# Kernel tuning notes

Hardware: AMD Instinct MI355X
Metric: run time of the kernel (lower is better)

The kernel has to match this reference:

```python
import jax, jax.numpy as jnp
import numpy as np

IOU_THRES = 0.45
NEG_POS_RATIO = 3
BBOX_XFORM_CLIP = float(np.log(1000.0 / 16.0))  # torchvision BoxCoder clamp


def _make_boxes(key, shape, img=512.0):
    # valid xyxy boxes inside a 512x512 image
    k1, k2 = jax.random.split(key)
    cxy = jax.random.uniform(k1, shape + (2,), minval=32.0, maxval=img - 32.0)
    wh = jax.random.uniform(k2, shape + (2,), minval=8.0, maxval=128.0)
    return jnp.concatenate([cxy - 0.5 * wh, cxy + 0.5 * wh], axis=-1)


def setup_inputs() -> dict:
    key = jax.random.key(0)
    B, A, G, C = 32, 32768, 64, 91
    ks = jax.random.split(key, 5)
    return {
        "cls_logits": jax.random.normal(ks[0], (B, A, C), dtype=jnp.float32),
        "bbox_regression": 0.1 * jax.random.normal(ks[1], (B, A, 4), dtype=jnp.float32),
        "anchors": _make_boxes(ks[2], (B, A)),
        "gt_boxes": _make_boxes(ks[3], (B, G)),
        "gt_labels": jax.random.randint(ks[4], (B, G), 0, C - 1),  # fg classes; C-1 is background
    }


def _pairwise_iou(boxes, anchors):
    # boxes [B,G,4] xyxy, anchors [B,A,4] xyxy -> [B,G,A]
    b = boxes[:, :, None, :]
    a = anchors[:, None, :, :]
    tl = jnp.maximum(b[..., :2], a[..., :2])
    br = jnp.minimum(b[..., 2:], a[..., 2:])
    wh = jnp.clip(br - tl, 0.0)
    inter = wh[..., 0] * wh[..., 1]
    area_b = (b[..., 2] - b[..., 0]) * (b[..., 3] - b[..., 1])
    area_a = (a[..., 2] - a[..., 0]) * (a[..., 3] - a[..., 1])
    return inter / (area_b + area_a - inter + 1e-16)


def _match(ious):
    # SSDMatcher: per-anchor best gt, threshold, then force best anchor per gt.
    # ious [G,A] -> matches [A] in {-1, 0..G-1}
    G = ious.shape[0]
    vals = ious.max(axis=0)
    m = jnp.argmax(ious, axis=0)
    m = jnp.where(vals < IOU_THRES, -1, m)
    best_anchor_per_gt = jnp.argmax(ious, axis=1)  # [G]
    return m.at[best_anchor_per_gt].set(jnp.arange(G))


def _decode(reg, anchors):
    # torchvision BoxCoder.decode_single, weights (1,1,1,1), xyxy anchors
    w = anchors[..., 2] - anchors[..., 0]
    h = anchors[..., 3] - anchors[..., 1]
    cx = anchors[..., 0] + 0.5 * w
    cy = anchors[..., 1] + 0.5 * h
    dx, dy, dw, dh = reg[..., 0], reg[..., 1], reg[..., 2], reg[..., 3]
    dw = jnp.minimum(dw, BBOX_XFORM_CLIP)
    dh = jnp.minimum(dh, BBOX_XFORM_CLIP)
    pcx = dx * w + cx
    pcy = dy * h + cy
    pw = jnp.exp(dw) * w
    ph = jnp.exp(dh) * h
    return jnp.stack([pcx - 0.5 * pw, pcy - 0.5 * ph, pcx + 0.5 * pw, pcy + 0.5 * ph], axis=-1)


def _giou_loss(pred, gt):
    # GIoU loss on xyxy boxes; elementwise over leading dims
    tl = jnp.maximum(pred[..., :2], gt[..., :2])
    br = jnp.minimum(pred[..., 2:], gt[..., 2:])
    wh = jnp.clip(br - tl, 0.0)
    inter = wh[..., 0] * wh[..., 1]
    ap = (pred[..., 2] - pred[..., 0]) * (pred[..., 3] - pred[..., 1])
    ag = (gt[..., 2] - gt[..., 0]) * (gt[..., 3] - gt[..., 1])
    union = ap + ag - inter + 1e-16
    iou = inter / union
    ctl = jnp.minimum(pred[..., :2], gt[..., :2])
    cbr = jnp.maximum(pred[..., 2:], gt[..., 2:])
    cwh = cbr - ctl
    ac = cwh[..., 0] * cwh[..., 1]
    giou = iou - (ac - union) / jnp.clip(ac, 1e-16)
    return 1.0 - jnp.clip(giou, -1.0, 1.0)


def reference(cls_logits, bbox_regression, anchors, gt_boxes, gt_labels):
    B, A, C = cls_logits.shape
    # --- matching ---
    ious = _pairwise_iou(gt_boxes, anchors)        # [B,G,A]
    matched = jax.vmap(_match)(ious)               # [B,A]
    fg = matched >= 0                              # [B,A]
    idx = jnp.clip(matched, 0)
    num_fg = fg.sum()
    # --- bbox loss (sum over foreground only, via masking) ---
    matched_gt = jnp.take_along_axis(gt_boxes, idx[..., None], axis=1)  # [B,A,4]
    pred = _decode(bbox_regression, anchors)                            # [B,A,4]
    bbox_loss_sum = jnp.sum(_giou_loss(pred, matched_gt) * fg)
    # --- classification targets + CE ---
    matched_lbl = jnp.take_along_axis(gt_labels, idx, axis=1)           # [B,A]
    cls_targets = jnp.where(fg, matched_lbl, C - 1)
    logp = jax.nn.log_softmax(cls_logits, axis=-1)
    cls_loss = -jnp.take_along_axis(logp, cls_targets[..., None], axis=-1)[..., 0]  # [B,A]
    neg_loss = jnp.where(fg, -jnp.inf, cls_loss)
    order = jnp.argsort(-neg_loss, axis=1)         # descending
    rank = jnp.argsort(order, axis=1)
    num_neg = NEG_POS_RATIO * fg.sum(axis=1, keepdims=True)
    bg = rank < num_neg
    # --- normalize ---
    N = jnp.maximum(1, num_fg).astype(cls_loss.dtype)
    bbox_loss = 2.0 * bbox_loss_sum / N
    cls_total = (jnp.sum(cls_loss * fg) + jnp.sum(cls_loss * bg)) / N
    return jnp.stack([bbox_loss, cls_total])  # [bbox_loss, cls_loss]
```

## Files before the change

### kernel.cpp

```cpp
#include <hip/hip_runtime.h>
#include <hip/hip_bf16.h>

#define B 32
#define A 32768
#define G 64
#define C 91
#define NBINS 2048

typedef unsigned long long ull;

static constexpr size_t offMatched = 0;
static constexpr size_t offBits    = (size_t)B * A * 4;
static constexpr size_t offNumFg   = (size_t)2 * B * A * 4;
static constexpr size_t offAcc     = offNumFg + B * 4;
static constexpr size_t offTick    = offAcc + 3 * 8;
static constexpr size_t offGt      = offTick + 8;
static constexpr int    ZERO_N     = (int)((offGt - offNumFg) / 4);

__global__ void init_kernel(int* zero_base, ull* gtpack) {
  int i = blockIdx.x * 256 + threadIdx.x;
  if (i < ZERO_N) zero_base[i] = 0;
  if (i < B * G) gtpack[i] = 0xFFFFFFFFull;
}

__global__ __launch_bounds__(256) void match_kernel(
    const float4* __restrict__ anchors, const float4* __restrict__ gt_boxes,
    int* __restrict__ matched, ull* __restrict__ gtpack) {
#pragma clang fp contract(off)
  int b = blockIdx.y;
  int a = blockIdx.x * 256 + threadIdx.x;
  __shared__ float4 gtb[G];
  __shared__ float gtarea[G];
  __shared__ ull best[G];
  if (threadIdx.x < G) {
    float4 g = gt_boxes[b * G + threadIdx.x];
    gtb[threadIdx.x] = g;
    gtarea[threadIdx.x] = (g.z - g.x) * (g.w - g.y);
    best[threadIdx.x] = 0ull;
  }
  __syncthreads();
  const unsigned* besthi = (const unsigned*)best;
  float4 an = anchors[(size_t)b * A + a];
  float area_a = (an.z - an.x) * (an.w - an.y);
  const unsigned lo = ~(unsigned)a;
  float bestv = -1.0f;
  int bestg = 0;
#pragma unroll 4
  for (int g = 0; g < G; ++g) {
    float4 gb = gtb[g];
    float tlx = fmaxf(gb.x, an.x), tly = fmaxf(gb.y, an.y);
    float brx = fminf(gb.z, an.z), bry = fminf(gb.w, an.w);
    float w = fmaxf(brx - tlx, 0.0f), h = fmaxf(bry - tly, 0.0f);
    float inter = w * h;
    if (inter > 0.0f) {
      float iou = inter / (gtarea[g] + area_a - inter + 1e-16f);
      if (iou > bestv) { bestv = iou; bestg = g; }
      unsigned ib = __float_as_uint(iou);
      if (ib >= besthi[2 * g + 1])
        atomicMax(&best[g], ((ull)ib << 32) | lo);
    }
  }
  matched[(size_t)b * A + a] = (bestv < 0.45f) ? -1 : bestg;
  __syncthreads();
  if (threadIdx.x < G) {
    ull p = best[threadIdx.x];
    if (p) atomicMax(&gtpack[b * G + threadIdx.x], p);
  }
}

__global__ void force_kernel(const ull* __restrict__ gtpack, int* __restrict__ matched) {
  int b = blockIdx.x * blockDim.x + threadIdx.x;
  if (b < B) {
    for (int g = 0; g < G; ++g) {
      unsigned a = ~(unsigned)(gtpack[b * G + g] & 0xFFFFFFFFull);
      matched[(size_t)b * A + a] = g;
    }
  }
}

#define APB 64
#define NT 8
#define NF4 (APB * C / 4)
#define NSTG 6
#define TAILN (NF4 - (NSTG - 1) * 256)

__device__ __forceinline__ void stage_tile(const float4* src, float* dst, int tid) {
  int wbase = tid & ~63;
#pragma unroll
  for (int r = 0; r < NSTG - 1; ++r)
    __builtin_amdgcn_global_load_lds(
        (const __attribute__((address_space(1))) void*)(src + r * 256 + tid),
        (__attribute__((address_space(3))) void*)(dst + (r * 256 + wbase) * 4),
        16, 0, 0);
  if (tid < TAILN)
    __builtin_amdgcn_global_load_lds(
        (const __attribute__((address_space(1))) void*)(src + (NSTG - 1) * 256 + tid),
        (__attribute__((address_space(3))) void*)(dst + ((NSTG - 1) * 256 + wbase) * 4),
        16, 0, 0);
}

__global__ __launch_bounds__(256) void loss_kernel(
    const float4* __restrict__ logit4, const float4* __restrict__ reg,
    const float4* __restrict__ anchors, const float4* __restrict__ gt_boxes,
    const int* __restrict__ gt_labels, const int* __restrict__ matched,
    unsigned* __restrict__ cls_bits, int* __restrict__ num_fg, double* __restrict__ acc) {
  __shared__ float buf[2][APB * C];
  __shared__ double rb[4], rf[4];
  __shared__ int rc[4];
  int tid = threadIdx.x;
  int b = blockIdx.y;
  int tile0 = blockIdx.x * NT;
  size_t bbase4 = (size_t)b * A * C / 4;
  int t4 = tid >> 2, q = tid & 3;

  int mm[NT], tcls[NT];
#pragma unroll
  for (int t = 0; t < NT; ++t) {
    mm[t] = matched[(size_t)b * A + (tile0 + t) * APB + t4];
    tcls[t] = (mm[t] >= 0) ? gt_labels[b * G + mm[t]] : (C - 1);
  }

  stage_tile(logit4 + bbase4 + (size_t)tile0 * NF4, buf[0], tid);
  stage_tile(logit4 + bbase4 + (size_t)(tile0 + 1) * NF4, buf[1], tid);

  double bbs = 0.0, fgs = 0.0;
  int cnt = 0;

#pragma unroll
  for (int t = 0; t < NT; ++t) {
    if (t < NT - 1) {
      asm volatile("s_waitcnt vmcnt(5)" ::: "memory");
    } else {
      asm volatile("s_waitcnt vmcnt(0)" ::: "memory");
    }
    __builtin_amdgcn_s_barrier();
    __builtin_amdgcn_sched_barrier(0);
    {
      const float* BC = buf[t & 1];
      int a = (tile0 + t) * APB + t4;
      const float* row = BC + t4 * C + 23 * q;
      const int cn = (q < 3) ? 23 : 22;
      float s0 = 0.f, s1 = 0.f, s2 = 0.f, s3 = 0.f;
      int j = 0;
#pragma unroll
      for (; j + 4 <= 20; j += 4) {
        s0 += __expf(row[j]);
        s1 += __expf(row[j + 1]);
        s2 += __expf(row[j + 2]);
        s3 += __expf(row[j + 3]);
      }
      for (; j < cn; ++j) s0 += __expf(row[j]);
      float s = (s0 + s1) + (s2 + s3);
      s += __shfl_xor(s, 1);
      s += __shfl_xor(s, 2);
      float lse = __logf(s);
      float xt = BC[t4 * C + tcls[t]];
      float loss = lse - xt;
      if (q == 0) {
        cls_bits[(size_t)b * A + a] = (mm[t] >= 0) ? 0u : __float_as_uint(loss);
        if (mm[t] >= 0) {
          fgs += (double)loss;
          cnt++;
          float4 an = anchors[(size_t)b * A + a];
          float4 rg = reg[(size_t)b * A + a];
          float4 gb = gt_boxes[b * G + mm[t]];
          float w = an.z - an.x, h = an.w - an.y;
          float cx = an.x + 0.5f * w, cy = an.y + 0.5f * h;
          float dw = fminf(rg.z, 4.135166556742356f);
          float dh = fminf(rg.w, 4.135166556742356f);
          float pcx = rg.x * w + cx, pcy = rg.y * h + cy;
          float pw = expf(dw) * w, ph = expf(dh) * h;
          float px0 = pcx - 0.5f * pw, py0 = pcy - 0.5f * ph;
          float px1 = pcx + 0.5f * pw, py1 = pcy + 0.5f * ph;
          float tlx = fmaxf(px0, gb.x), tly = fmaxf(py0, gb.y);
          float brx = fminf(px1, gb.z), bry = fminf(py1, gb.w);
          float iw = fmaxf(brx - tlx, 0.f), ih = fmaxf(bry - tly, 0.f);
          float inter = iw * ih;
          float ap = (px1 - px0) * (py1 - py0);
          float ag = (gb.z - gb.x) * (gb.w - gb.y);
          float uni = ap + ag - inter + 1e-16f;
          float iou = inter / uni;
          float ctlx = fminf(px0, gb.x), ctly = fminf(py0, gb.y);
          float cbrx = fmaxf(px1, gb.z), cbry = fmaxf(py1, gb.w);
          float acr = (cbrx - ctlx) * (cbry - ctly);
          float giou = iou - (acr - uni) / fmaxf(acr, 1e-16f);
          giou = fminf(fmaxf(giou, -1.f), 1.f);
          bbs += (double)(1.f - giou);
        }
      }
    }
    __builtin_amdgcn_s_barrier();
    __builtin_amdgcn_sched_barrier(0);
    if (t + 2 < NT)
      stage_tile(logit4 + bbase4 + (size_t)(tile0 + t + 2) * NF4, buf[t & 1], tid);
  }

  int lane = tid & 63, wave = tid >> 6;
  for (int o = 32; o; o >>= 1) {
    bbs += __shfl_xor(bbs, o);
    fgs += __shfl_xor(fgs, o);
    cnt += __shfl_xor(cnt, o);
  }
  if (lane == 0) { rb[wave] = bbs; rf[wave] = fgs; rc[wave] = cnt; }
  __syncthreads();
  if (tid == 0) {
    double tb = rb[0] + rb[1] + rb[2] + rb[3];
    double tf = rf[0] + rf[1] + rf[2] + rf[3];
    int tc = rc[0] + rc[1] + rc[2] + rc[3];
    if (tb != 0.0) atomicAdd(&acc[0], tb);
    if (tf != 0.0) atomicAdd(&acc[1], tf);
    if (tc) atomicAdd(&num_fg[b], tc);
  }
}

__global__ __launch_bounds__(1024) void select_fused(
    const unsigned* __restrict__ bits, const int* __restrict__ num_fg,
    double* __restrict__ acc, int* __restrict__ ticket, float* __restrict__ out) {
  int b = blockIdx.x, tid = threadIdx.x;
  __shared__ int h[NBINS];
  __shared__ int gsum[256];
  __shared__ float sT;
  __shared__ int sDone, sKrem, sR;
  __shared__ unsigned sPref;
  __shared__ double sd[16];

  unsigned bv[32];
#pragma unroll
  for (int i = 0; i < 32; ++i) bv[i] = bits[(size_t)b * A + i * 1024 + tid];
  if (tid == 0) { sDone = 0; sR = 0; }

  for (int i = tid; i < NBINS; i += 1024) h[i] = 0;
  __syncthreads();
#pragma unroll
  for (int i = 0; i < 32; ++i) atomicAdd(&h[bv[i] >> 21], 1);
  __syncthreads();
  if (tid < 256) {
    int gs = 0;
#pragma unroll
    for (int j = 0; j < 8; ++j) gs += h[tid * 8 + j];
    gsum[tid] = gs;
  }
  __syncthreads();
  if (tid == 0) {
    int nf = num_fg[b];
    int k = 3 * nf;
    int bgcnt = A - nf;
    if (k <= 0) { sT = __builtin_inff(); sDone = 1; }
    else if (k >= bgcnt) { sT = -1.0f; sDone = 1; }
    else {
      int run = 0, gidx = 255;
      for (; gidx >= 0; --gidx) { if (run + gsum[gidx] >= k) break; run += gsum[gidx]; }
      if (gidx < 0) { sT = -1.0f; sDone = 1; }
      else {
        int bin = gidx * 8 + 7;
        for (; bin > gidx * 8; --bin) { if (run + h[bin] >= k) break; run += h[bin]; }
        sPref = (unsigned)bin; sKrem = k - run;
      }
    }
  }
  __syncthreads();

  if (!sDone) {
    unsigned p1 = sPref;
    int k = sKrem;
    __syncthreads();
    for (int i = tid; i < NBINS; i += 1024) h[i] = 0;
    __syncthreads();
#pragma unroll
    for (int i = 0; i < 32; ++i)
      if ((bv[i] >> 21) == p1) atomicAdd(&h[(bv[i] >> 10) & 2047], 1);
    __syncthreads();
    if (tid < 256) {
      int gs = 0;
#pragma unroll
      for (int j = 0; j < 8; ++j) gs += h[tid * 8 + j];
      gsum[tid] = gs;
    }
    __syncthreads();
    if (tid == 0) {
      int run = 0, gidx = 255;
      for (; gidx >= 0; --gidx) { if (run + gsum[gidx] >= k) break; run += gsum[gidx]; }
      if (gidx < 0) { sT = -1.0f; sDone = 1; }
      else {
        int bin = gidx * 8 + 7;
        for (; bin > gidx * 8; --bin) { if (run + h[bin] >= k) break; run += h[bin]; }
        sPref = (p1 << 11) | (unsigned)bin; sKrem = k - run;
      }
    }
    __syncthreads();
  }
  if (!sDone) {
    unsigned p2 = sPref;
    int k = sKrem;
    __syncthreads();
    if (tid < 1024) h[tid] = 0;
    __syncthreads();
#pragma unroll
    for (int i = 0; i < 32; ++i)
      if ((bv[i] >> 10) == p2) atomicAdd(&h[bv[i] & 1023], 1);
    __syncthreads();
    if (tid < 256) {
      int gs = 0;
#pragma unroll
      for (int j = 0; j < 4; ++j) gs += h[tid * 4 + j];
      gsum[tid] = gs;
    }
    __syncthreads();
    if (tid == 0) {
      int run = 0, gidx = 255;
      for (; gidx >= 0; --gidx) { if (run + gsum[gidx] >= k) break; run += gsum[gidx]; }
      if (gidx < 0) { sT = -1.0f; }
      else {
        int bin = gidx * 4 + 3;
        for (; bin > gidx * 4; --bin) { if (run + h[bin] >= k) break; run += h[bin]; }
        sT = __uint_as_float((p2 << 10) | (unsigned)bin);
        sR = k - run;
      }
    }
    __syncthreads();
  }

  float T = sT;
  float ls = 0.f;
#pragma unroll
  for (int i = 0; i < 32; ++i) {
    float v = __uint_as_float(bv[i]);
    if (v > T) ls += v;
  }
  for (int o = 32; o; o >>= 1) ls += __shfl_xor(ls, o);
  if ((tid & 63) == 0) sd[tid >> 6] = (double)ls;
  __syncthreads();
  if (tid == 0) {
    double tt = 0.0;
    for (int w = 0; w < 16; ++w) tt += sd[w];
    if (sR > 0) tt += (double)sR * (double)sT;
    if (tt != 0.0) atomicAdd(&acc[2], tt);
    __threadfence();
    if (atomicAdd(ticket, 1) == B - 1) {
      int tot = 0;
      for (int bb = 0; bb < B; ++bb) tot += num_fg[bb];
      double N = (double)(tot > 1 ? tot : 1);
      double a2 = atomicAdd(&acc[2], 0.0);
      out[0] = (float)(2.0 * acc[0] / N);
      out[1] = (float)((acc[1] + a2) / N);
    }
  }
}

extern "C" void kernel_launch(void* const* d_in, const int* in_sizes, int n_in,
                              void* d_out, int out_size, void* d_ws, size_t ws_size,
                              hipStream_t stream) {
  const float4* logit4  = (const float4*)d_in[0];
  const float4* reg     = (const float4*)d_in[1];
  const float4* anchors = (const float4*)d_in[2];
  const float4* gtb     = (const float4*)d_in[3];
  const int*    gtl     = (const int*)d_in[4];

  char* ws = (char*)d_ws;
  int*      matched = (int*)(ws + offMatched);
  unsigned* cbits   = (unsigned*)(ws + offBits);
  int*      numfg   = (int*)(ws + offNumFg);
  double*   acc     = (double*)(ws + offAcc);
  int*      tick    = (int*)(ws + offTick);
  ull*      gtpack  = (ull*)(ws + offGt);
  float*    out     = (float*)d_out;

  init_kernel<<<8, 256, 0, stream>>>((int*)(ws + offNumFg), gtpack);
  match_kernel<<<dim3(A / 256, B), 256, 0, stream>>>(anchors, gtb, matched, gtpack);
  force_kernel<<<1, 64, 0, stream>>>(gtpack, matched);
  loss_kernel<<<dim3(A / (APB * NT), B), 256, 0, stream>>>(
      logit4, reg, anchors, gtb, gtl, matched, cbits, numfg, acc);
  select_fused<<<B, 1024, 0, stream>>>(cbits, numfg, acc, tick + 1, out);
}
```

Measured before the change: 705.5 us.

## Fuse anchor matching into loss kernel and patch forced matches in a fixup pass

Removes the separate match and force kernels and computes each anchor's IoU matching inside the loss kernel, with four lanes per anchor splitting the 64 gt boxes and combining results by shuffle. Forced best-anchor-per-gt matches are then applied afterwards by a small fixup kernel that recomputes the logsumexp and GIoU for those anchors and adds delta corrections to the accumulators. The aim is to avoid a full extra pass over the anchors, the matched-index round trip and two kernel launches. In exchange the loss pipeline drops from double-buffered prefetch two tiles ahead to one tile ahead, adds matching compute and LDS atomics inside the logit streaming loop, and introduces a delta-correction scheme for forced matches that could introduce subtle ordering or duplicate-handling differences.

```diff
diff --git a/kernel.cpp b/kernel.cpp
--- a/kernel.cpp
+++ b/kernel.cpp
@@ -23,59 +23,85 @@
   if (i < B * G) gtpack[i] = 0xFFFFFFFFull;
 }
 
-__global__ __launch_bounds__(256) void match_kernel(
-    const float4* __restrict__ anchors, const float4* __restrict__ gt_boxes,
-    int* __restrict__ matched, ull* __restrict__ gtpack) {
+__device__ __forceinline__ float giou_term(float4 an, float4 rg, float4 gb) {
 #pragma clang fp contract(off)
-  int b = blockIdx.y;
-  int a = blockIdx.x * 256 + threadIdx.x;
-  __shared__ float4 gtb[G];
-  __shared__ float gtarea[G];
-  __shared__ ull best[G];
-  if (threadIdx.x < G) {
-    float4 g = gt_boxes[b * G + threadIdx.x];
-    gtb[threadIdx.x] = g;
-    gtarea[threadIdx.x] = (g.z - g.x) * (g.w - g.y);
-    best[threadIdx.x] = 0ull;
-  }
-  __syncthreads();
-  const unsigned* besthi = (const unsigned*)best;
-  float4 an = anchors[(size_t)b * A + a];
+  float w = an.z - an.x, h = an.w - an.y;
+  float cx = an.x + 0.5f * w, cy = an.y + 0.5f * h;
+  float dw = fminf(rg.z, 4.135166556742356f);
+  float dh = fminf(rg.w, 4.135166556742356f);
+  float pcx = rg.x * w + cx, pcy = rg.y * h + cy;
+  float pw = expf(dw) * w, ph = expf(dh) * h;
+  float px0 = pcx - 0.5f * pw, py0 = pcy - 0.5f * ph;
+  float px1 = pcx + 0.5f * pw, py1 = pcy + 0.5f * ph;
+  float tlx = fmaxf(px0, gb.x), tly = fmaxf(py0, gb.y);
+  float brx = fminf(px1, gb.z), bry = fminf(py1, gb.w);
+  float iw = fmaxf(brx - tlx, 0.f), ih = fmaxf(bry - tly, 0.f);
+  float inter = iw * ih;
+  float ap = (px1 - px0) * (py1 - py0);
+  float ag = (gb.z - gb.x) * (gb.w - gb.y);
+  float uni = ap + ag - inter + 1e-16f;
+  float iou = inter / uni;
+  float ctlx = fminf(px0, gb.x), ctly = fminf(py0, gb.y);
+  float cbrx = fmaxf(px1, gb.z), cbry = fmaxf(py1, gb.w);
+  float acr = (cbrx - ctlx) * (cbry - ctly);
+  float giou = iou - (acr - uni) / fmaxf(acr, 1e-16f);
+  giou = fminf(fmaxf(giou, -1.f), 1.f);
+  return 1.f - giou;
+}
+
+__device__ __forceinline__ float lse_replay(const float* row) {
+#pragma clang fp contract(off)
+  float sq[4];
+#pragma unroll
+  for (int q = 0; q < 4; ++q) {
+    const float* r = row + 23 * q;
+    const int cn = (q < 3) ? 23 : 22;
+    float s0 = 0.f, s1 = 0.f, s2 = 0.f, s3 = 0.f;
+    int j = 0;
+    for (; j + 4 <= 20; j += 4) {
+      s0 += __expf(r[j]);
+      s1 += __expf(r[j + 1]);
+      s2 += __expf(r[j + 2]);
+      s3 += __expf(r[j + 3]);
+    }
+    for (; j < cn; ++j) s0 += __expf(r[j]);
+    sq[q] = (s0 + s1) + (s2 + s3);
+  }
+  return __logf((sq[0] + sq[1]) + (sq[2] + sq[3]));
+}
+
+__device__ __forceinline__ void inline_match(
+    const float4* __restrict__ anchors_b, const float4* gtb, const float* gtarea,
+    ull* bestl, const int* __restrict__ gtl_b, int aidx, int q, int& mm, int& tcl) {
+#pragma clang fp contract(off)
+  float4 an = anchors_b[aidx];
   float area_a = (an.z - an.x) * (an.w - an.y);
-  const unsigned lo = ~(unsigned)a;
+  const unsigned lo = ~(unsigned)aidx;
+  const unsigned* besthi = (const unsigned*)bestl;
   float bestv = -1.0f;
   int bestg = 0;
+  const int g0 = q * 16;
 #pragma unroll 4
-  for (int g = 0; g < G; ++g) {
+  for (int g = g0; g < g0 + 16; ++g) {
     float4 gb = gtb[g];
     float tlx = fmaxf(gb.x, an.x), tly = fmaxf(gb.y, an.y);
     float brx = fminf(gb.z, an.z), bry = fminf(gb.w, an.w);
     float w = fmaxf(brx - tlx, 0.0f), h = fmaxf(bry - tly, 0.0f);
     float inter = w * h;
+    float iou = 0.0f;
     if (inter > 0.0f) {
-      float iou = inter / (gtarea[g] + area_a - inter + 1e-16f);
-      if (iou > bestv) { bestv = iou; bestg = g; }
+      iou = inter / (gtarea[g] + area_a - inter + 1e-16f);
       unsigned ib = __float_as_uint(iou);
-      if (ib >= besthi[2 * g + 1])
-        atomicMax(&best[g], ((ull)ib << 32) | lo);
-    }
-  }
-  matched[(size_t)b * A + a] = (bestv < 0.45f) ? -1 : bestg;
-  __syncthreads();
-  if (threadIdx.x < G) {
-    ull p = best[threadIdx.x];
-    if (p) atomicMax(&gtpack[b * G + threadIdx.x], p);
-  }
-}
-
-__global__ void force_kernel(const ull* __restrict__ gtpack, int* __restrict__ matched) {
-  int b = blockIdx.x * blockDim.x + threadIdx.x;
-  if (b < B) {
-    for (int g = 0; g < G; ++g) {
-      unsigned a = ~(unsigned)(gtpack[b * G + g] & 0xFFFFFFFFull);
-      matched[(size_t)b * A + a] = g;
-    }
-  }
+      if (ib >= besthi[2 * g + 1]) atomicMax(&bestl[g], ((ull)ib << 32) | lo);
+    }
+    if (iou > bestv) { bestv = iou; bestg = g; }
+  }
+  ull p = ((ull)__float_as_uint(bestv) << 32) | (unsigned)(G - 1 - bestg);
+  ull p1 = __shfl_xor(p, 1); p = (p > p1) ? p : p1;
+  ull p2 = __shfl_xor(p, 2); p = (p > p2) ? p : p2;
+  float bv = __uint_as_float((unsigned)(p >> 32));
+  mm = (bv < 0.45f) ? -1 : (G - 1 - (int)(p & 0xFFFFFFFFull));
+  tcl = (mm >= 0) ? gtl_b[mm] : (C - 1);
 }
 
 #define APB 64
@@ -99,42 +125,49 @@
         16, 0, 0);
 }
 
-__global__ __launch_bounds__(256) void loss_kernel(
+__global__ __launch_bounds__(256) void fused_loss_kernel(
     const float4* __restrict__ logit4, const float4* __restrict__ reg,
     const float4* __restrict__ anchors, const float4* __restrict__ gt_boxes,
-    const int* __restrict__ gt_labels, const int* __restrict__ matched,
-    unsigned* __restrict__ cls_bits, int* __restrict__ num_fg, double* __restrict__ acc) {
+    const int* __restrict__ gt_labels, int* __restrict__ matched,
+    unsigned* __restrict__ cls_bits, int* __restrict__ num_fg,
+    double* __restrict__ acc, ull* __restrict__ gtpack) {
   __shared__ float buf[2][APB * C];
+  __shared__ float4 gtb[G];
+  __shared__ float gtarea[G];
+  __shared__ ull bestl[G];
   __shared__ double rb[4], rf[4];
   __shared__ int rc[4];
   int tid = threadIdx.x;
   int b = blockIdx.y;
   int tile0 = blockIdx.x * NT;
   size_t bbase4 = (size_t)b * A * C / 4;
+  size_t abase = (size_t)b * A;
+  const float4* anchors_b = anchors + abase;
+  const int* gtl_b = gt_labels + b * G;
   int t4 = tid >> 2, q = tid & 3;
 
-  int mm[NT], tcls[NT];
-#pragma unroll
-  for (int t = 0; t < NT; ++t) {
-    mm[t] = matched[(size_t)b * A + (tile0 + t) * APB + t4];
-    tcls[t] = (mm[t] >= 0) ? gt_labels[b * G + mm[t]] : (C - 1);
-  }
-
+  if (tid < G) {
+    float4 g = gt_boxes[b * G + tid];
+    gtb[tid] = g;
+    gtarea[tid] = (g.z - g.x) * (g.w - g.y);
+    bestl[tid] = 0ull;
+  }
   stage_tile(logit4 + bbase4 + (size_t)tile0 * NF4, buf[0], tid);
-  stage_tile(logit4 + bbase4 + (size_t)(tile0 + 1) * NF4, buf[1], tid);
+  __syncthreads();
+
+  int mm, tcl;
+  inline_match(anchors_b, gtb, gtarea, bestl, gtl_b, tile0 * APB + t4, q, mm, tcl);
 
   double bbs = 0.0, fgs = 0.0;
   int cnt = 0;
 
-#pragma unroll
   for (int t = 0; t < NT; ++t) {
-    if (t < NT - 1) {
-      asm volatile("s_waitcnt vmcnt(5)" ::: "memory");
-    } else {
-      asm volatile("s_waitcnt vmcnt(0)" ::: "memory");
-    }
-    __builtin_amdgcn_s_barrier();
-    __builtin_amdgcn_sched_barrier(0);
+    if (t + 1 < NT)
+      stage_tile(logit4 + bbase4 + (size_t)(tile0 + t + 1) * NF4, buf[(t + 1) & 1], tid);
+    int mmN = 0, tclN = 0;
+    if (t + 1 < NT)
+      inline_match(anchors_b, gtb, gtarea, bestl, gtl_b,
+                   (tile0 + t + 1) * APB + t4, q, mmN, tclN);
     {
       const float* BC = buf[t & 1];
       int a = (tile0 + t) * APB + t4;
@@ -154,45 +187,28 @@
       s += __shfl_xor(s, 1);
       s += __shfl_xor(s, 2);
       float lse = __logf(s);
-      float xt = BC[t4 * C + tcls[t]];
+      float xt = BC[t4 * C + tcl];
       float loss = lse - xt;
       if (q == 0) {
-        cls_bits[(size_t)b * A + a] = (mm[t] >= 0) ? 0u : __float_as_uint(loss);
-        if (mm[t] >= 0) {
+        matched[abase + a] = mm;
+        cls_bits[abase + a] = (mm >= 0) ? 0u : __float_as_uint(loss);
+        if (mm >= 0) {
           fgs += (double)loss;
           cnt++;
-          float4 an = anchors[(size_t)b * A + a];
-          float4 rg = reg[(size_t)b * A + a];
-          float4 gb = gt_boxes[b * G + mm[t]];
-          float w = an.z - an.x, h = an.w - an.y;
-          float cx = an.x + 0.5f * w, cy = an.y + 0.5f * h;
-          float dw = fminf(rg.z, 4.135166556742356f);
-          float dh = fminf(rg.w, 4.135166556742356f);
-          float pcx = rg.x * w + cx, pcy = rg.y * h + cy;
-          float pw = expf(dw) * w, ph = expf(dh) * h;
-          float px0 = pcx - 0.5f * pw, py0 = pcy - 0.5f * ph;
-          float px1 = pcx + 0.5f * pw, py1 = pcy + 0.5f * ph;
-          float tlx = fmaxf(px0, gb.x), tly = fmaxf(py0, gb.y);
-          float brx = fminf(px1, gb.z), bry = fminf(py1, gb.w);
-          float iw = fmaxf(brx - tlx, 0.f), ih = fmaxf(bry - tly, 0.f);
-          float inter = iw * ih;
-          float ap = (px1 - px0) * (py1 - py0);
-          float ag = (gb.z - gb.x) * (gb.w - gb.y);
-          float uni = ap + ag - inter + 1e-16f;
-          float iou = inter / uni;
-          float ctlx = fminf(px0, gb.x), ctly = fminf(py0, gb.y);
-          float cbrx = fmaxf(px1, gb.z), cbry = fmaxf(py1, gb.w);
-          float acr = (cbrx - ctlx) * (cbry - ctly);
-          float giou = iou - (acr - uni) / fmaxf(acr, 1e-16f);
-          giou = fminf(fmaxf(giou, -1.f), 1.f);
-          bbs += (double)(1.f - giou);
+          float4 an = anchors_b[a];
+          float4 rg = reg[abase + a];
+          bbs += (double)giou_term(an, rg, gtb[mm]);
         }
       }
     }
-    __builtin_amdgcn_s_barrier();
-    __builtin_amdgcn_sched_barrier(0);
-    if (t + 2 < NT)
-      stage_tile(logit4 + bbase4 + (size_t)(tile0 + t + 2) * NF4, buf[t & 1], tid);
+    mm = mmN;
+    tcl = tclN;
+    __syncthreads();
+  }
+
+  if (tid < G) {
+    ull p = bestl[tid];
+    if (p) atomicMax(&gtpack[b * G + tid], p);
   }
 
   int lane = tid & 63, wave = tid >> 6;
@@ -210,6 +226,51 @@
     if (tb != 0.0) atomicAdd(&acc[0], tb);
     if (tf != 0.0) atomicAdd(&acc[1], tf);
     if (tc) atomicAdd(&num_fg[b], tc);
+  }
+}
+
+__global__ __launch_bounds__(64) void fixup_kernel(
+    const float* __restrict__ logits, const float4* __restrict__ reg,
+    const float4* __restrict__ anchors, const float4* __restrict__ gt_boxes,
+    const int* __restrict__ gt_labels, const ull* __restrict__ gtpack,
+    const int* __restrict__ matched, unsigned* __restrict__ cls_bits,
+    int* __restrict__ num_fg, double* __restrict__ acc) {
+  int b = blockIdx.x, g = threadIdx.x;
+  __shared__ unsigned aArr[G];
+  unsigned a = ~(unsigned)(gtpack[b * G + g] & 0xFFFFFFFFull);
+  aArr[g] = a;
+  __syncthreads();
+  bool winner = true;
+  for (int g2 = g + 1; g2 < G; ++g2)
+    if (aArr[g2] == a) { winner = false; break; }
+
+  double d_bb = 0.0, d_fg = 0.0;
+  int d_cnt = 0;
+  int m_old = matched[(size_t)b * A + a];
+  if (winner && m_old != g) {
+    const float* row = logits + ((size_t)b * A + a) * C;
+    float lse = lse_replay(row);
+    float4 an = anchors[(size_t)b * A + a];
+    float4 rg = reg[(size_t)b * A + a];
+    if (m_old >= 0) {
+      d_fg -= (double)(lse - row[gt_labels[b * G + m_old]]);
+      d_bb -= (double)giou_term(an, rg, gt_boxes[b * G + m_old]);
+    } else {
+      cls_bits[(size_t)b * A + a] = 0u;
+      d_cnt = 1;
+    }
+    d_fg += (double)(lse - row[gt_labels[b * G + g]]);
+    d_bb += (double)giou_term(an, rg, gt_boxes[b * G + g]);
+  }
+  for (int o = 32; o; o >>= 1) {
+    d_bb += __shfl_xor(d_bb, o);
+    d_fg += __shfl_xor(d_fg, o);
+    d_cnt += __shfl_xor(d_cnt, o);
+  }
+  if (g == 0) {
+    if (d_bb != 0.0) atomicAdd(&acc[0], d_bb);
+    if (d_fg != 0.0) atomicAdd(&acc[1], d_fg);
+    if (d_cnt) atomicAdd(&num_fg[b], d_cnt);
   }
 }
 
@@ -366,9 +427,9 @@
   float*    out     = (float*)d_out;
 
   init_kernel<<<8, 256, 0, stream>>>((int*)(ws + offNumFg), gtpack);
-  match_kernel<<<dim3(A / 256, B), 256, 0, stream>>>(anchors, gtb, matched, gtpack);
-  force_kernel<<<1, 64, 0, stream>>>(gtpack, matched);
-  loss_kernel<<<dim3(A / (APB * NT), B), 256, 0, stream>>>(
-      logit4, reg, anchors, gtb, gtl, matched, cbits, numfg, acc);
+  fused_loss_kernel<<<dim3(A / (APB * NT), B), 256, 0, stream>>>(
+      logit4, reg, anchors, gtb, gtl, matched, cbits, numfg, acc, gtpack);
+  fixup_kernel<<<B, 64, 0, stream>>>(
+      (const float*)d_in[0], reg, anchors, gtb, gtl, gtpack, matched, cbits, numfg, acc);
   select_fused<<<B, 1024, 0, stream>>>(cbits, numfg, acc, tick + 1, out);
 }
```

New measurement: 627.3 us. 11.1% less time.
